# Optimization experiments

Hardware: AMD Instinct MI355X
Metric: run time of the kernel (lower is better)

Reference implementation:

```python
import jax, jax.numpy as jnp
import numpy as np

N_BUCKET, EPB, EMBED, K, TAU = 64, 8, 1024, 2, 1.0
EPS_NORM, EPS_W = 1e-12, 1e-9

def _l2norm(x):
    n = jnp.linalg.norm(x, axis=-1, keepdims=True)
    return x / jnp.maximum(n, EPS_NORM)

def setup_inputs() -> dict:
    key = jax.random.key(0)
    k1, k2, k3 = jax.random.split(key, 3)
    h = jax.random.normal(k1, (8, 2048, EMBED), dtype=jnp.float32)
    op_id = jax.random.randint(k2, (8, 2048), 0, N_BUCKET, dtype=jnp.int64)
    expert_key = jax.random.normal(k3, (N_BUCKET, EPB, EMBED), dtype=jnp.float32) / np.sqrt(EMBED)
    return {"h": h, "op_id": op_id, "expert_key": expert_key}

def reference(h, op_id, expert_key):
    # h: (B,T,C), op_id: (B,T), expert_key: (n_bucket, epb, C)
    bucket = jnp.clip(op_id, 0, N_BUCKET - 1)          # (B,T)
    h_n = _l2norm(h)                                    # (B,T,C)
    keys = _l2norm(expert_key)                          # (nb,epb,C)
    keys_bt = keys[bucket]                              # gather -> (B,T,epb,C)
    score = jnp.einsum('btc,btec->bte', h_n, keys_bt)   # (B,T,epb)
    score = score / max(TAU, 1e-6)
    probs_local = jax.nn.softmax(score, axis=-1)        # (B,T,epb)
    topv, local = jax.lax.top_k(probs_local, K)         # (B,T,k) each
    w = topv / (jnp.sum(topv, axis=-1, keepdims=True) + EPS_W)
    gid = bucket[..., None] * EPB + local               # (B,T,k) global expert ids
    return (gid, w)
```

## Files before the change

### kernel.cpp

```cpp
#include <hip/hip_runtime.h>
#include <cmath>

#define EMBED   1024
#define EPB     8
#define NB      64
#define KTOP    2
#define TPW     8

__global__ __launch_bounds__(1024) void bin_kernel(
    const int* __restrict__ op, int ntok,
    int* __restrict__ bstart_g, int* __restrict__ cnt_g,
    int* __restrict__ cpre_g, int* __restrict__ chunk2b,
    int* __restrict__ perm) {
    __shared__ int s_hist[NB];
    __shared__ int s_cur[NB];
    int tid = threadIdx.x, lane = tid & 63;
    if (tid < NB) s_hist[tid] = 0;
    __syncthreads();
    for (int i = tid; i < ntok; i += 1024) {
        int b = min(max(op[i], 0), NB - 1);
        atomicAdd(&s_hist[b], 1);
    }
    __syncthreads();
    if (tid < 64) {
        int c   = s_hist[tid];
        int nch = (c + TPW - 1) / TPW;
        int ic = c, in = nch;
#pragma unroll
        for (int off = 1; off < 64; off <<= 1) {
            int vc = __shfl_up(ic, off, 64);
            int vn = __shfl_up(in, off, 64);
            if (lane >= off) { ic += vc; in += vn; }
        }
        int bs = ic - c;
        int cp = in - nch;
        s_cur[tid]    = bs;
        bstart_g[tid] = bs;
        cnt_g[tid]    = c;
        cpre_g[tid]   = cp;
        if (tid == 63) cpre_g[NB] = in;
        for (int j = 0; j < nch; ++j) chunk2b[cp + j] = tid;
    }
    __syncthreads();
    for (int i = tid; i < ntok; i += 1024) {
        int b = min(max(op[i], 0), NB - 1);
        int pos = atomicAdd(&s_cur[b], 1);
        perm[pos] = i;
    }
}

#define LOADK(e) \
    float4 k##e##_0 = kb[(e)*256 +       lane]; \
    float4 k##e##_1 = kb[(e)*256 +  64 + lane]; \
    float4 k##e##_2 = kb[(e)*256 + 128 + lane]; \
    float4 k##e##_3 = kb[(e)*256 + 192 + lane];

#define SQE(e) \
    float s##e = k##e##_0.x*k##e##_0.x + k##e##_0.y*k##e##_0.y + k##e##_0.z*k##e##_0.z + k##e##_0.w*k##e##_0.w; \
    s##e += k##e##_1.x*k##e##_1.x + k##e##_1.y*k##e##_1.y + k##e##_1.z*k##e##_1.z + k##e##_1.w*k##e##_1.w; \
    s##e += k##e##_2.x*k##e##_2.x + k##e##_2.y*k##e##_2.y + k##e##_2.z*k##e##_2.z + k##e##_2.w*k##e##_2.w; \
    s##e += k##e##_3.x*k##e##_3.x + k##e##_3.y*k##e##_3.y + k##e##_3.z*k##e##_3.z + k##e##_3.w*k##e##_3.w;

#define REDS(off) \
    s0 += __shfl_xor(s0, off, 64); s1 += __shfl_xor(s1, off, 64); \
    s2 += __shfl_xor(s2, off, 64); s3 += __shfl_xor(s3, off, 64); \
    s4 += __shfl_xor(s4, off, 64); s5 += __shfl_xor(s5, off, 64); \
    s6 += __shfl_xor(s6, off, 64); s7 += __shfl_xor(s7, off, 64);

#define ACC1(e,c) \
    d##e += hv##c.x * k##e##_##c.x + hv##c.y * k##e##_##c.y + \
            hv##c.z * k##e##_##c.z + hv##c.w * k##e##_##c.w;

#define STEP_C(c) \
    hh += hv##c.x*hv##c.x + hv##c.y*hv##c.y + hv##c.z*hv##c.z + hv##c.w*hv##c.w; \
    ACC1(0,c) ACC1(1,c) ACC1(2,c) ACC1(3,c) \
    ACC1(4,c) ACC1(5,c) ACC1(6,c) ACC1(7,c)

#define REDD(off) \
    hh += __shfl_xor(hh, off, 64); \
    d0 += __shfl_xor(d0, off, 64); d1 += __shfl_xor(d1, off, 64); \
    d2 += __shfl_xor(d2, off, 64); d3 += __shfl_xor(d3, off, 64); \
    d4 += __shfl_xor(d4, off, 64); d5 += __shfl_xor(d5, off, 64); \
    d6 += __shfl_xor(d6, off, 64); d7 += __shfl_xor(d7, off, 64);

#define T1(e) if (ex##e > v1) { v1 = ex##e; i1 = (e); }
#define T2(e) if ((e) != i1 && ex##e > v2) { v2 = ex##e; i2 = (e); }

__global__ __launch_bounds__(64, 2) void router_regkey_kernel(
    const float* __restrict__ h, const float* __restrict__ ek,
    const int* __restrict__ perm, const int* __restrict__ bstart_g,
    const int* __restrict__ cnt_g, const int* __restrict__ cpre_g,
    const int* __restrict__ chunk2b,
    float* __restrict__ out_gid, float* __restrict__ out_w) {
    int wid  = blockIdx.x;
    int lane = threadIdx.x;
    int total = cpre_g[NB];
    if (wid >= total) return;

    int b    = chunk2b[wid];
    int lc   = wid - cpre_g[b];
    int base = bstart_g[b] + lc * TPW;
    int end  = bstart_g[b] + cnt_g[b];

    const float4* kb = (const float4*)ek + (size_t)b * (EPB * EMBED / 4);
    LOADK(0) LOADK(1) LOADK(2) LOADK(3) LOADK(4) LOADK(5) LOADK(6) LOADK(7)

    SQE(0) SQE(1) SQE(2) SQE(3) SQE(4) SQE(5) SQE(6) SQE(7)
    REDS(32) REDS(16) REDS(8) REDS(4) REDS(2) REDS(1)
    float rke0 = 1.0f / fmaxf(sqrtf(s0), 1e-12f);
    float rke1 = 1.0f / fmaxf(sqrtf(s1), 1e-12f);
    float rke2 = 1.0f / fmaxf(sqrtf(s2), 1e-12f);
    float rke3 = 1.0f / fmaxf(sqrtf(s3), 1e-12f);
    float rke4 = 1.0f / fmaxf(sqrtf(s4), 1e-12f);
    float rke5 = 1.0f / fmaxf(sqrtf(s5), 1e-12f);
    float rke6 = 1.0f / fmaxf(sqrtf(s6), 1e-12f);
    float rke7 = 1.0f / fmaxf(sqrtf(s7), 1e-12f);

    int tok[TPW];
#pragma unroll
    for (int t = 0; t < TPW; ++t) tok[t] = perm[min(base + t, end - 1)];

#pragma unroll
    for (int t = 0; t < TPW; ++t) {
        const float4* hrow = (const float4*)(h + (size_t)tok[t] * EMBED);
        float4 hv0 = hrow[lane];
        float4 hv1 = hrow[ 64 + lane];
        float4 hv2 = hrow[128 + lane];
        float4 hv3 = hrow[192 + lane];

        float hh = 0.f;
        float d0 = 0.f, d1 = 0.f, d2 = 0.f, d3 = 0.f;
        float d4 = 0.f, d5 = 0.f, d6 = 0.f, d7 = 0.f;
        STEP_C(0) STEP_C(1) STEP_C(2) STEP_C(3)

        REDD(32) REDD(16) REDD(8) REDD(4) REDD(2) REDD(1)

        float rh = 1.0f / fmaxf(sqrtf(hh), 1e-12f);
        float sc0 = d0 * rh * rke0, sc1 = d1 * rh * rke1;
        float sc2 = d2 * rh * rke2, sc3 = d3 * rh * rke3;
        float sc4 = d4 * rh * rke4, sc5 = d5 * rh * rke5;
        float sc6 = d6 * rh * rke6, sc7 = d7 * rh * rke7;
        float m = -1e30f;
        m = fmaxf(m, sc0); m = fmaxf(m, sc1); m = fmaxf(m, sc2); m = fmaxf(m, sc3);
        m = fmaxf(m, sc4); m = fmaxf(m, sc5); m = fmaxf(m, sc6); m = fmaxf(m, sc7);
        float ex0 = expf(sc0 - m), ex1 = expf(sc1 - m);
        float ex2 = expf(sc2 - m), ex3 = expf(sc3 - m);
        float ex4 = expf(sc4 - m), ex5 = expf(sc5 - m);
        float ex6 = expf(sc6 - m), ex7 = expf(sc7 - m);
        float Z = 0.f;
        Z += ex0; Z += ex1; Z += ex2; Z += ex3;
        Z += ex4; Z += ex5; Z += ex6; Z += ex7;

        float v1 = ex0; int i1 = 0;
        T1(1) T1(2) T1(3) T1(4) T1(5) T1(6) T1(7)
        float v2 = (i1 == 0) ? ex1 : ex0;
        int   i2 = (i1 == 0) ? 1 : 0;
        T2(0) T2(1) T2(2) T2(3) T2(4) T2(5) T2(6) T2(7)

        if (lane == 0 && (base + t) < end) {
            float p1 = v1 / Z;
            float p2 = v2 / Z;
            float ws = p1 + p2 + 1e-9f;
            int tk = tok[t];
            ((float2*)out_gid)[tk] =
                make_float2((float)(b * EPB + i1), (float)(b * EPB + i2));
            ((float2*)out_w)[tk] = make_float2(p1 / ws, p2 / ws);
        }
    }
}

__global__ void key_rnorm_kernel(const float* __restrict__ ek,
                                 float* __restrict__ rnorm) {
    int wave = (int)((blockIdx.x * blockDim.x + threadIdx.x) >> 6);
    int lane = threadIdx.x & 63;
    if (wave >= NB * EPB) return;
    const float4* row = (const float4*)(ek + (size_t)wave * EMBED);
    float s = 0.f;
#pragma unroll
    for (int c = 0; c < 4; ++c) {
        float4 v = row[c * 64 + lane];
        s += v.x * v.x + v.y * v.y + v.z * v.z + v.w * v.w;
    }
#pragma unroll
    for (int off = 32; off; off >>= 1) s += __shfl_xor(s, off, 64);
    if (lane == 0) rnorm[wave] = 1.0f / fmaxf(sqrtf(s), 1e-12f);
}

__global__ __launch_bounds__(256, 6) void router_duo_kernel(
    const float* __restrict__ h, const int* __restrict__ op,
    const float* __restrict__ ek, const float* __restrict__ rk,
    float* __restrict__ out_gid, float* __restrict__ out_w, int ntok) {
    int gtid = blockIdx.x * blockDim.x + threadIdx.x;
    int wid  = gtid >> 6;
    int lane = threadIdx.x & 63;
    int half = lane >> 5;
    int r    = lane & 31;
    int tq   = wid * 2 + half;
    int tc   = min(tq, ntok - 1);

    int b = op[tc];
    b = min(max(b, 0), NB - 1);

    const float4* hrow = (const float4*)(h + (size_t)tc * EMBED);
    const float4* kb   = (const float4*)ek + (size_t)b * (EPB * EMBED / 4);

    float dot[EPB] = {0.f, 0.f, 0.f, 0.f, 0.f, 0.f, 0.f, 0.f};
    float hh = 0.f;
#pragma unroll
    for (int i = 0; i < 8; ++i) {
        float4 a = hrow[i * 32 + r];
        hh += a.x * a.x + a.y * a.y + a.z * a.z + a.w * a.w;
#pragma unroll
        for (int e = 0; e < EPB; ++e) {
            float4 kvv = kb[e * 256 + i * 32 + r];
            dot[e] += a.x * kvv.x + a.y * kvv.y + a.z * kvv.z + a.w * kvv.w;
        }
    }
#pragma unroll
    for (int off = 16; off; off >>= 1) {
        hh += __shfl_xor(hh, off, 64);
#pragma unroll
        for (int e = 0; e < EPB; ++e) dot[e] += __shfl_xor(dot[e], off, 64);
    }
    float rh = 1.0f / fmaxf(sqrtf(hh), 1e-12f);
    float sc[EPB];
    float m = -1e30f;
#pragma unroll
    for (int e = 0; e < EPB; ++e) {
        sc[e] = dot[e] * rh * rk[b * EPB + e];
        m = fmaxf(m, sc[e]);
    }
    float ex[EPB];
    float Z = 0.f;
#pragma unroll
    for (int e = 0; e < EPB; ++e) { ex[e] = expf(sc[e] - m); Z += ex[e]; }
    int i1 = 0;
#pragma unroll
    for (int e = 1; e < EPB; ++e) if (ex[e] > ex[i1]) i1 = e;
    int i2 = (i1 == 0) ? 1 : 0;
#pragma unroll
    for (int e = 0; e < EPB; ++e)
        if (e != i1 && ex[e] > ex[i2]) i2 = e;
    if (r == 0 && tq < ntok) {
        float p1 = ex[i1] / Z;
        float p2 = ex[i2] / Z;
        float ws = p1 + p2 + 1e-9f;
        ((float2*)out_gid)[tq] =
            make_float2((float)(b * EPB + i1), (float)(b * EPB + i2));
        ((float2*)out_w)[tq] = make_float2(p1 / ws, p2 / ws);
    }
}

extern "C" void kernel_launch(void* const* d_in, const int* in_sizes, int n_in,
                              void* d_out, int out_size, void* d_ws, size_t ws_size,
                              hipStream_t stream) {
    const float* h     = (const float*)d_in[0];
    const int*   op_id = (const int*)  d_in[1];
    const float* ek    = (const float*)d_in[2];

    int ntok  = in_sizes[1];
    int maxch = NB + (ntok + TPW - 1) / TPW;

    float* out_gid = (float*)d_out;
    float* out_w   = out_gid + (size_t)ntok * KTOP;

    float* rk      = (float*)d_ws;
    int*   bstart  = (int*)(rk + 512);
    int*   cnt     = bstart + NB;
    int*   cpre    = cnt + NB;
    int*   chunk2b = cpre + (NB + 1);
    int*   perm    = chunk2b + maxch;
    size_t need    = ((size_t)(512 + 2 * NB + NB + 1 + maxch) + (size_t)ntok) * 4;

    if (ws_size < need) {
        key_rnorm_kernel<<<128, 256, 0, stream>>>(ek, rk);
        int blocks2 = (ntok + 7) / 8;
        router_duo_kernel<<<blocks2, 256, 0, stream>>>(h, op_id, ek, rk,
                                                       out_gid, out_w, ntok);
        return;
    }

    bin_kernel<<<1, 1024, 0, stream>>>(op_id, ntok, bstart, cnt, cpre,
                                       chunk2b, perm);
    router_regkey_kernel<<<maxch, 64, 0, stream>>>(
        h, ek, perm, bstart, cnt, cpre, chunk2b, out_gid, out_w);
}
```

Measured before the change: 131.1 us.

## Parallelize token binning across blocks and double-buffer hidden-row loads in router

Splits the single-block binning kernel into a multi-block histogram, a one-wave scan and a multi-block scatter that uses global atomics. This is meant to cut the serial latency of one 1024-thread block walking all tokens. The router now packs four waves per 256-thread block and software-pipelines the eight token rows with A/B register buffers, so the next row's load overlaps the current dot products. Empty asm statements pin the key registers. The cost is extra kernel launches plus a memset, and higher register pressure from the double buffer.

```diff
diff --git a/kernel.cpp b/kernel.cpp
--- a/kernel.cpp
+++ b/kernel.cpp
@@ -7,44 +7,52 @@
 #define KTOP    2
 #define TPW     8
 
-__global__ __launch_bounds__(1024) void bin_kernel(
-    const int* __restrict__ op, int ntok,
-    int* __restrict__ bstart_g, int* __restrict__ cnt_g,
-    int* __restrict__ cpre_g, int* __restrict__ chunk2b,
-    int* __restrict__ perm) {
-    __shared__ int s_hist[NB];
-    __shared__ int s_cur[NB];
-    int tid = threadIdx.x, lane = tid & 63;
-    if (tid < NB) s_hist[tid] = 0;
+__global__ void hist_kernel(const int* __restrict__ op, int ntok,
+                            int* __restrict__ count) {
+    __shared__ int hc[NB];
+    int tid = threadIdx.x;
+    if (tid < NB) hc[tid] = 0;
     __syncthreads();
-    for (int i = tid; i < ntok; i += 1024) {
+    for (int i = blockIdx.x * blockDim.x + tid; i < ntok;
+         i += gridDim.x * blockDim.x) {
         int b = min(max(op[i], 0), NB - 1);
-        atomicAdd(&s_hist[b], 1);
+        atomicAdd(&hc[b], 1);
     }
     __syncthreads();
-    if (tid < 64) {
-        int c   = s_hist[tid];
-        int nch = (c + TPW - 1) / TPW;
-        int ic = c, in = nch;
-#pragma unroll
-        for (int off = 1; off < 64; off <<= 1) {
-            int vc = __shfl_up(ic, off, 64);
-            int vn = __shfl_up(in, off, 64);
-            if (lane >= off) { ic += vc; in += vn; }
-        }
-        int bs = ic - c;
-        int cp = in - nch;
-        s_cur[tid]    = bs;
-        bstart_g[tid] = bs;
-        cnt_g[tid]    = c;
-        cpre_g[tid]   = cp;
-        if (tid == 63) cpre_g[NB] = in;
-        for (int j = 0; j < nch; ++j) chunk2b[cp + j] = tid;
-    }
-    __syncthreads();
-    for (int i = tid; i < ntok; i += 1024) {
+    if (tid < NB && hc[tid]) atomicAdd(&count[tid], hc[tid]);
+}
+
+__global__ void scan_kernel(const int* __restrict__ count,
+                            int* __restrict__ bstart,
+                            int* __restrict__ soffs,
+                            int* __restrict__ cpre,
+                            int* __restrict__ chunk2b) {
+    int tid = threadIdx.x;
+    int c   = count[tid];
+    int nch = (c + TPW - 1) / TPW;
+    int ic = c, in = nch;
+#pragma unroll
+    for (int off = 1; off < 64; off <<= 1) {
+        int vc = __shfl_up(ic, off, 64);
+        int vn = __shfl_up(in, off, 64);
+        if (tid >= off) { ic += vc; in += vn; }
+    }
+    int bs = ic - c;
+    int cp = in - nch;
+    bstart[tid] = bs;
+    soffs[tid]  = bs;
+    cpre[tid]   = cp;
+    if (tid == 63) cpre[NB] = in;
+    for (int j = 0; j < nch; ++j) chunk2b[cp + j] = tid;
+}
+
+__global__ void scatter_kernel(const int* __restrict__ op, int ntok,
+                               int* __restrict__ soffs,
+                               int* __restrict__ perm) {
+    for (int i = blockIdx.x * blockDim.x + threadIdx.x; i < ntok;
+         i += gridDim.x * blockDim.x) {
         int b = min(max(op[i], 0), NB - 1);
-        int pos = atomicAdd(&s_cur[b], 1);
+        int pos = atomicAdd(&soffs[b], 1);
         perm[pos] = i;
     }
 }
@@ -55,6 +63,9 @@
     float4 k##e##_2 = kb[(e)*256 + 128 + lane]; \
     float4 k##e##_3 = kb[(e)*256 + 192 + lane];
 
+#define PIN4(v) asm volatile("" : "+v"(v.x), "+v"(v.y), "+v"(v.z), "+v"(v.w))
+#define PINK(e) PIN4(k##e##_0); PIN4(k##e##_1); PIN4(k##e##_2); PIN4(k##e##_3);
+
 #define SQE(e) \
     float s##e = k##e##_0.x*k##e##_0.x + k##e##_0.y*k##e##_0.y + k##e##_0.z*k##e##_0.z + k##e##_0.w*k##e##_0.w; \
     s##e += k##e##_1.x*k##e##_1.x + k##e##_1.y*k##e##_1.y + k##e##_1.z*k##e##_1.z + k##e##_1.w*k##e##_1.w; \
@@ -67,14 +78,19 @@
     s4 += __shfl_xor(s4, off, 64); s5 += __shfl_xor(s5, off, 64); \
     s6 += __shfl_xor(s6, off, 64); s7 += __shfl_xor(s7, off, 64);
 
-#define ACC1(e,c) \
-    d##e += hv##c.x * k##e##_##c.x + hv##c.y * k##e##_##c.y + \
-            hv##c.z * k##e##_##c.z + hv##c.w * k##e##_##c.w;
-
-#define STEP_C(c) \
-    hh += hv##c.x*hv##c.x + hv##c.y*hv##c.y + hv##c.z*hv##c.z + hv##c.w*hv##c.w; \
-    ACC1(0,c) ACC1(1,c) ACC1(2,c) ACC1(3,c) \
-    ACC1(4,c) ACC1(5,c) ACC1(6,c) ACC1(7,c)
+#define LOADH(P, tk) { \
+    const float4* hrow_ = (const float4*)(h + (size_t)(tk) * EMBED); \
+    h##P##0 = hrow_[lane];       h##P##1 = hrow_[ 64 + lane]; \
+    h##P##2 = hrow_[128 + lane]; h##P##3 = hrow_[192 + lane]; }
+
+#define ACC1(e, c, P) \
+    d##e += h##P##c.x * k##e##_##c.x + h##P##c.y * k##e##_##c.y + \
+            h##P##c.z * k##e##_##c.z + h##P##c.w * k##e##_##c.w;
+
+#define STEPC(c, P) \
+    hh += h##P##c.x*h##P##c.x + h##P##c.y*h##P##c.y + h##P##c.z*h##P##c.z + h##P##c.w*h##P##c.w; \
+    ACC1(0,c,P) ACC1(1,c,P) ACC1(2,c,P) ACC1(3,c,P) \
+    ACC1(4,c,P) ACC1(5,c,P) ACC1(6,c,P) ACC1(7,c,P)
 
 #define REDD(off) \
     hh += __shfl_xor(hh, off, 64); \
@@ -86,14 +102,50 @@
 #define T1(e) if (ex##e > v1) { v1 = ex##e; i1 = (e); }
 #define T2(e) if ((e) != i1 && ex##e > v2) { v2 = ex##e; i2 = (e); }
 
-__global__ __launch_bounds__(64, 2) void router_regkey_kernel(
+#define BODY(P, t) { \
+    float hh = 0.f; \
+    float d0 = 0.f, d1 = 0.f, d2 = 0.f, d3 = 0.f; \
+    float d4 = 0.f, d5 = 0.f, d6 = 0.f, d7 = 0.f; \
+    STEPC(0,P) STEPC(1,P) STEPC(2,P) STEPC(3,P) \
+    REDD(32) REDD(16) REDD(8) REDD(4) REDD(2) REDD(1) \
+    float rh = 1.0f / fmaxf(sqrtf(hh), 1e-12f); \
+    float sc0 = d0 * rh * rke0, sc1 = d1 * rh * rke1; \
+    float sc2 = d2 * rh * rke2, sc3 = d3 * rh * rke3; \
+    float sc4 = d4 * rh * rke4, sc5 = d5 * rh * rke5; \
+    float sc6 = d6 * rh * rke6, sc7 = d7 * rh * rke7; \
+    float m = -1e30f; \
+    m = fmaxf(m, sc0); m = fmaxf(m, sc1); m = fmaxf(m, sc2); m = fmaxf(m, sc3); \
+    m = fmaxf(m, sc4); m = fmaxf(m, sc5); m = fmaxf(m, sc6); m = fmaxf(m, sc7); \
+    float ex0 = expf(sc0 - m), ex1 = expf(sc1 - m); \
+    float ex2 = expf(sc2 - m), ex3 = expf(sc3 - m); \
+    float ex4 = expf(sc4 - m), ex5 = expf(sc5 - m); \
+    float ex6 = expf(sc6 - m), ex7 = expf(sc7 - m); \
+    float Z = 0.f; \
+    Z += ex0; Z += ex1; Z += ex2; Z += ex3; \
+    Z += ex4; Z += ex5; Z += ex6; Z += ex7; \
+    float v1 = ex0; int i1 = 0; \
+    T1(1) T1(2) T1(3) T1(4) T1(5) T1(6) T1(7) \
+    float v2 = (i1 == 0) ? ex1 : ex0; \
+    int   i2 = (i1 == 0) ? 1 : 0; \
+    T2(0) T2(1) T2(2) T2(3) T2(4) T2(5) T2(6) T2(7) \
+    if (lane == 0 && (base + (t)) < end) { \
+        float p1 = v1 / Z; \
+        float p2 = v2 / Z; \
+        float ws = p1 + p2 + 1e-9f; \
+        int tk = tok[t]; \
+        ((float2*)out_gid)[tk] = \
+            make_float2((float)(b * EPB + i1), (float)(b * EPB + i2)); \
+        ((float2*)out_w)[tk] = make_float2(p1 / ws, p2 / ws); \
+    } }
+
+__global__ __launch_bounds__(256, 2) void router_regkey_kernel(
     const float* __restrict__ h, const float* __restrict__ ek,
     const int* __restrict__ perm, const int* __restrict__ bstart_g,
     const int* __restrict__ cnt_g, const int* __restrict__ cpre_g,
     const int* __restrict__ chunk2b,
     float* __restrict__ out_gid, float* __restrict__ out_w) {
-    int wid  = blockIdx.x;
-    int lane = threadIdx.x;
+    int wid  = (int)((blockIdx.x * blockDim.x + threadIdx.x) >> 6);
+    int lane = threadIdx.x & 63;
     int total = cpre_g[NB];
     if (wid >= total) return;
 
@@ -104,6 +156,7 @@
 
     const float4* kb = (const float4*)ek + (size_t)b * (EPB * EMBED / 4);
     LOADK(0) LOADK(1) LOADK(2) LOADK(3) LOADK(4) LOADK(5) LOADK(6) LOADK(7)
+    PINK(0) PINK(1) PINK(2) PINK(3) PINK(4) PINK(5) PINK(6) PINK(7)
 
     SQE(0) SQE(1) SQE(2) SQE(3) SQE(4) SQE(5) SQE(6) SQE(7)
     REDS(32) REDS(16) REDS(8) REDS(4) REDS(2) REDS(1)
@@ -120,53 +173,17 @@
 #pragma unroll
     for (int t = 0; t < TPW; ++t) tok[t] = perm[min(base + t, end - 1)];
 
-#pragma unroll
-    for (int t = 0; t < TPW; ++t) {
-        const float4* hrow = (const float4*)(h + (size_t)tok[t] * EMBED);
-        float4 hv0 = hrow[lane];
-        float4 hv1 = hrow[ 64 + lane];
-        float4 hv2 = hrow[128 + lane];
-        float4 hv3 = hrow[192 + lane];
-
-        float hh = 0.f;
-        float d0 = 0.f, d1 = 0.f, d2 = 0.f, d3 = 0.f;
-        float d4 = 0.f, d5 = 0.f, d6 = 0.f, d7 = 0.f;
-        STEP_C(0) STEP_C(1) STEP_C(2) STEP_C(3)
-
-        REDD(32) REDD(16) REDD(8) REDD(4) REDD(2) REDD(1)
-
-        float rh = 1.0f / fmaxf(sqrtf(hh), 1e-12f);
-        float sc0 = d0 * rh * rke0, sc1 = d1 * rh * rke1;
-        float sc2 = d2 * rh * rke2, sc3 = d3 * rh * rke3;
-        float sc4 = d4 * rh * rke4, sc5 = d5 * rh * rke5;
-        float sc6 = d6 * rh * rke6, sc7 = d7 * rh * rke7;
-        float m = -1e30f;
-        m = fmaxf(m, sc0); m = fmaxf(m, sc1); m = fmaxf(m, sc2); m = fmaxf(m, sc3);
-        m = fmaxf(m, sc4); m = fmaxf(m, sc5); m = fmaxf(m, sc6); m = fmaxf(m, sc7);
-        float ex0 = expf(sc0 - m), ex1 = expf(sc1 - m);
-        float ex2 = expf(sc2 - m), ex3 = expf(sc3 - m);
-        float ex4 = expf(sc4 - m), ex5 = expf(sc5 - m);
-        float ex6 = expf(sc6 - m), ex7 = expf(sc7 - m);
-        float Z = 0.f;
-        Z += ex0; Z += ex1; Z += ex2; Z += ex3;
-        Z += ex4; Z += ex5; Z += ex6; Z += ex7;
-
-        float v1 = ex0; int i1 = 0;
-        T1(1) T1(2) T1(3) T1(4) T1(5) T1(6) T1(7)
-        float v2 = (i1 == 0) ? ex1 : ex0;
-        int   i2 = (i1 == 0) ? 1 : 0;
-        T2(0) T2(1) T2(2) T2(3) T2(4) T2(5) T2(6) T2(7)
-
-        if (lane == 0 && (base + t) < end) {
-            float p1 = v1 / Z;
-            float p2 = v2 / Z;
-            float ws = p1 + p2 + 1e-9f;
-            int tk = tok[t];
-            ((float2*)out_gid)[tk] =
-                make_float2((float)(b * EPB + i1), (float)(b * EPB + i2));
-            ((float2*)out_w)[tk] = make_float2(p1 / ws, p2 / ws);
-        }
-    }
+    float4 hA0, hA1, hA2, hA3;
+    float4 hB0, hB1, hB2, hB3;
+    LOADH(A, tok[0])
+    LOADH(B, tok[1])  BODY(A, 0)
+    LOADH(A, tok[2])  BODY(B, 1)
+    LOADH(B, tok[3])  BODY(A, 2)
+    LOADH(A, tok[4])  BODY(B, 3)
+    LOADH(B, tok[5])  BODY(A, 4)
+    LOADH(A, tok[6])  BODY(B, 5)
+    LOADH(B, tok[7])  BODY(A, 6)
+    BODY(B, 7)
 }
 
 __global__ void key_rnorm_kernel(const float* __restrict__ ek,
@@ -265,12 +282,13 @@
     float* out_w   = out_gid + (size_t)ntok * KTOP;
 
     float* rk      = (float*)d_ws;
-    int*   bstart  = (int*)(rk + 512);
-    int*   cnt     = bstart + NB;
-    int*   cpre    = cnt + NB;
+    int*   count   = (int*)(rk + 512);
+    int*   bstart  = count  + NB;
+    int*   soffs   = bstart + NB;
+    int*   cpre    = soffs  + NB;
     int*   chunk2b = cpre + (NB + 1);
     int*   perm    = chunk2b + maxch;
-    size_t need    = ((size_t)(512 + 2 * NB + NB + 1 + maxch) + (size_t)ntok) * 4;
+    size_t need    = ((size_t)(512 + 3 * NB + NB + 1 + maxch) + (size_t)ntok) * 4;
 
     if (ws_size < need) {
         key_rnorm_kernel<<<128, 256, 0, stream>>>(ek, rk);
@@ -280,8 +298,11 @@
         return;
     }
 
-    bin_kernel<<<1, 1024, 0, stream>>>(op_id, ntok, bstart, cnt, cpre,
-                                       chunk2b, perm);
-    router_regkey_kernel<<<maxch, 64, 0, stream>>>(
-        h, ek, perm, bstart, cnt, cpre, chunk2b, out_gid, out_w);
-}
+    hipMemsetAsync(count, 0, NB * sizeof(int), stream);
+    hist_kernel<<<16, 256, 0, stream>>>(op_id, ntok, count);
+    scan_kernel<<<1, 64, 0, stream>>>(count, bstart, soffs, cpre, chunk2b);
+    scatter_kernel<<<16, 256, 0, stream>>>(op_id, ntok, soffs, perm);
+    int blocks = (maxch * 64 + 255) / 256;
+    router_regkey_kernel<<<blocks, 256, 0, stream>>>(
+        h, ek, perm, bstart, count, cpre, chunk2b, out_gid, out_w);
+}
```

Measured after the change: 159.6 us. +21.8%, slower.
